# Kernel optimization log

Hardware: AMD Instinct MI355X
Metric: run time of the kernel (lower is better)

## Reference

```python
import jax, jax.numpy as jnp
import numpy as np

K = 16                 # nn_k neighbors (self excluded)
FILTER_SCALE = 2.0
SHARPNESS_SIGMA = 0.75
EPS = 1e-17


def _eps_denom(x):
    return jnp.where(x < EPS, EPS, x)


def _normalize(x):
    # F.normalize(dim=-1) semantics
    return x / jnp.maximum(jnp.linalg.norm(x, axis=-1, keepdims=True), 1e-12)


def _gather(feat, idx):
    # feat: (B,P,D), idx: (B,P,K) -> (B,P,K,D)   (== pytorch3d knn_gather)
    return jnp.take_along_axis(feat[:, None, :, :], idx[:, :, :, None], axis=2)


def _knn(points, k):
    # points: (B,P,3) -> squared dists (B,P,k), idxs (B,P,k); self excluded
    d2 = jnp.sum(points * points, axis=-1)
    dists = d2[:, :, None] + d2[:, None, :] - 2.0 * jnp.einsum('bpd,bqd->bpq', points, points)
    P = points.shape[1]
    r = jnp.arange(P)
    dists = dists.at[:, r, r].set(-jnp.inf)  # force self to be rank-0 of top_k
    neg, idx = jax.lax.top_k(-dists, k + 1)
    return jnp.maximum(-neg[:, :, 1:], 0.0), idx[:, :, 1:]


def _denoise(normals, idx, w):
    # weighted neighbor average of normals, per _denoise_normals
    nn_n = _gather(normals, idx)                       # (B,P,K,3)
    return jnp.sum(nn_n * w[..., None], axis=-2) / _eps_denom(
        jnp.sum(w, axis=-1, keepdims=True))


def setup_inputs() -> dict:
    key = jax.random.key(0)
    kp, kn = jax.random.split(key)
    B, P = 2, 8192
    points = jax.random.normal(kp, (B, P, 3), dtype=jnp.float32)
    normals = jax.random.normal(kn, (B, P, 3), dtype=jnp.float32)
    return {"points": points, "normals": normals}


def reference(points, normals):
    # --- torch.no_grad block: knn build + all weights + normal denoising ---
    pts_ng = jax.lax.stop_gradient(points)
    dists, idx = _knn(pts_ng, K)                       # (B,P,K)
    nn = _gather(pts_ng, idx)                          # (B,P,K,3), detached

    # phi = (1 - d/(2*d1*fs^2))^4, clamped at 0 (get_phi)
    s = dists[:, :, :1] * 2.0 * FILTER_SCALE * FILTER_SCALE
    w = jnp.maximum(1.0 - dists / _eps_denom(s), 0.0)
    phi = (w * w) * (w * w)

    n_ng = jax.lax.stop_gradient(normals)
    n1 = _denoise(n_ng, idx, phi)                      # first denoise with phi

    # normal_w = exp(-||n - ni||^2 / sigma^2) on normalized once-denoised normals
    nn_n = _gather(n1, idx)
    diff = _normalize(nn_n) - _normalize(n1)[:, :, None, :]
    inv_sigma = 1.0 / (SHARPNESS_SIGMA * SHARPNESS_SIGMA)
    normal_w = jnp.exp(-jnp.sum(diff * diff, axis=-1) * inv_sigma)

    # second denoise with phi * normal_w
    n2 = _denoise(n1, idx, phi * normal_w)

    # weights_proj = phi * spatial_w_proj(==1) * normal_w, ball-query masked
    weights_proj = phi * normal_w
    ball_mask = dists > FILTER_SCALE * dists[:, :, :1] * 2.0
    weights_proj = jnp.where(ball_mask, 0.0, weights_proj)
    weights_proj = jax.lax.stop_gradient(weights_proj)

    # --- outside no_grad: gather denoised normals, signed point-to-plane ---
    nn_normals = _gather(n2, idx)                      # (B,P,K,3) (no grad path)
    dist_to_surface = jnp.sum((nn - points[:, :, None, :]) * nn_normals, axis=-1)

    # projection loss: weighted mean of squared point-to-plane distance
    loss = jnp.sum(dist_to_surface * dist_to_surface * weights_proj, axis=-1) / \
        _eps_denom(jnp.sum(weights_proj, axis=-1))     # (B,P)
    return jnp.mean(loss)                              # BaseLoss reduction='mean'
```

## Files before the change

kernel.cpp:

```cpp
#include <hip/hip_runtime.h>
#include <math.h>

#define PP    8192
#define NB    2
#define NPTS  16384
#define KNN   16
#define EPSV  1e-17f
#define CH    128
#define NSUP  16
#define NCELL 4096

#define KEY_BIG 3.0e38f


__device__ __forceinline__ int spread3(int v) {
    return (v & 1) | ((v & 2) << 2) | ((v & 4) << 4) | ((v & 8) << 6);
}

__global__ __launch_bounds__(1024) void sort_kernel(
        const float* __restrict__ pts,
        float4* __restrict__ sorted4,
        int*    __restrict__ perm) {
    __shared__ int lh[NCELL];
    __shared__ int wtot[16];
    const int b = blockIdx.x;
    const int t = threadIdx.x;
    const int lane = t & 63, wid = t >> 6;
    const float* bp = pts + (size_t)b * PP * 3;

    for (int k = t; k < NCELL; k += 1024) lh[k] = 0;
    __syncthreads();

    float px[8], py[8], pz[8];
    int cell[8];
#pragma unroll
    for (int k = 0; k < 8; ++k) {
        const int p = t + k * 1024;
        const float x = bp[p * 3 + 0];
        const float y = bp[p * 3 + 1];
        const float z = bp[p * 3 + 2];
        px[k] = x; py[k] = y; pz[k] = z;
        const int ix = (int)fminf(fmaxf((x + 5.0f) * 1.6f, 0.0f), 15.0f);
        const int iy = (int)fminf(fmaxf((y + 5.0f) * 1.6f, 0.0f), 15.0f);
        const int iz = (int)fminf(fmaxf((z + 5.0f) * 1.6f, 0.0f), 15.0f);
        cell[k] = spread3(ix) | (spread3(iy) << 1) | (spread3(iz) << 2);
        atomicAdd(&lh[cell[k]], 1);
    }
    __syncthreads();

    const int v0 = lh[t * 4 + 0];
    const int v1 = lh[t * 4 + 1];
    const int v2 = lh[t * 4 + 2];
    const int v3 = lh[t * 4 + 3];
    const int s4 = v0 + v1 + v2 + v3;
    int v = s4;
#pragma unroll
    for (int off = 1; off < 64; off <<= 1) {
        int uu = __shfl_up(v, off, 64);
        if (lane >= off) v += uu;
    }
    if (lane == 63) wtot[wid] = v;
    __syncthreads();
    if (wid == 0) {
        int w = (lane < 16) ? wtot[lane] : 0;
#pragma unroll
        for (int off = 1; off < 16; off <<= 1) {
            int uu = __shfl_up(w, off, 64);
            if (lane >= off) w += uu;
        }
        if (lane < 16) wtot[lane] = w;
    }
    __syncthreads();
    const int wbase = (wid > 0) ? wtot[wid - 1] : 0;
    const int excl = wbase + v - s4;
    lh[t * 4 + 0] = excl;
    lh[t * 4 + 1] = excl + v0;
    lh[t * 4 + 2] = excl + v0 + v1;
    lh[t * 4 + 3] = excl + v0 + v1 + v2;
    __syncthreads();

#pragma unroll
    for (int k = 0; k < 8; ++k) {
        const int pos = atomicAdd(&lh[cell[k]], 1);
        sorted4[(size_t)b * PP + pos] =
            make_float4(px[k], py[k], pz[k],
                        px[k] * px[k] + py[k] * py[k] + pz[k] * pz[k]);
        perm[b * PP + pos] = t + k * 1024;
    }
}

__global__ void bbox_kernel(const float4* __restrict__ sorted4,
                            float4* __restrict__ bbmin,
                            float4* __restrict__ bbmax,
                            float4* __restrict__ sbmin,
                            float4* __restrict__ sbmax) {
    __shared__ float4 smn[8], smx[8];
    const int lane = threadIdx.x & 63;
    const int wave = threadIdx.x >> 6;
    const int cw = blockIdx.x * 8 + wave;
    const float4 v = sorted4[cw * 64 + lane];
    float mnx = v.x, mny = v.y, mnz = v.z;
    float mxx = v.x, mxy = v.y, mxz = v.z;
#pragma unroll
    for (int off = 32; off >= 1; off >>= 1) {
        mnx = fminf(mnx, __shfl_xor(mnx, off, 64));
        mny = fminf(mny, __shfl_xor(mny, off, 64));
        mnz = fminf(mnz, __shfl_xor(mnz, off, 64));
        mxx = fmaxf(mxx, __shfl_xor(mxx, off, 64));
        mxy = fmaxf(mxy, __shfl_xor(mxy, off, 64));
        mxz = fmaxf(mxz, __shfl_xor(mxz, off, 64));
    }
    if (lane == 0) {
        bbmin[cw] = make_float4(mnx, mny, mnz, 0.f);
        bbmax[cw] = make_float4(mxx, mxy, mxz, 0.f);
        smn[wave] = make_float4(mnx, mny, mnz, 0.f);
        smx[wave] = make_float4(mxx, mxy, mxz, 0.f);
    }
    __syncthreads();
    if (threadIdx.x == 0) {
        float4 a = smn[0], bmx = smx[0];
#pragma unroll
        for (int k = 1; k < 8; ++k) {
            a.x = fminf(a.x, smn[k].x); a.y = fminf(a.y, smn[k].y);
            a.z = fminf(a.z, smn[k].z);
            bmx.x = fmaxf(bmx.x, smx[k].x); bmx.y = fmaxf(bmx.y, smx[k].y);
            bmx.z = fmaxf(bmx.z, smx[k].z);
        }
        sbmin[blockIdx.x] = a;
        sbmax[blockIdx.x] = bmx;
    }
}

__device__ __forceinline__ void insert16(float (&keys)[KNN], float kk) {
#pragma unroll
    for (int s = KNN - 1; s >= 1; --s)
        keys[s] = __builtin_amdgcn_fmed3f(keys[s - 1], kk, keys[s]);
    keys[0] = fminf(keys[0], kk);
}

__device__ __forceinline__ void merge16(float (&a)[KNN], const float (&o)[KNN]) {
    float c[KNN];
#pragma unroll
    for (int s = 0; s < KNN; ++s) c[s] = fminf(a[s], o[KNN - 1 - s]);
#pragma unroll
    for (int st = KNN / 2; st >= 1; st >>= 1) {
#pragma unroll
        for (int base = 0; base < KNN; base += 2 * st) {
#pragma unroll
            for (int k = 0; k < st; ++k) {
                const float x = c[base + k], y = c[base + k + st];
                c[base + k]      = fminf(x, y);
                c[base + k + st] = fmaxf(x, y);
            }
        }
    }
#pragma unroll
    for (int s = 0; s < KNN; ++s) a[s] = c[s];
}

__global__ __launch_bounds__(256) void knn2_kernel(
        const float4* __restrict__ sorted4,
        const int*    __restrict__ perm,
        const float*  __restrict__ normals,
        const float4* __restrict__ bbmin,
        const float4* __restrict__ bbmax,
        const float4* __restrict__ sbmin,
        const float4* __restrict__ sbmax,
        int*   __restrict__ out_idx,
        float* __restrict__ out_phi,
        float* __restrict__ out_n1) {
    const int lane = threadIdx.x & 63;
    const int wv   = threadIdx.x >> 6;
    const int W    = blockIdx.x * 4 + wv;
    const int b    = W >> 12;
    const int qg   = W & 4095;
    const int qbase = qg * 2;
    const int i    = lane & 1;
    const int u    = lane >> 1;
    const int qloc = qbase + i;
    const int s0   = qbase >> 9;
    const float4* sb = sorted4 + (size_t)b * PP;
    const int bCH = b * CH;

    const float4 q4 = sb[qloc];
    const float qx = q4.x, qy = q4.y, qz = q4.z;
    const float d2q = qx * qx + qy * qy + qz * qz;

    float keys[KNN];
#pragma unroll
    for (int s = 0; s < KNN; ++s) keys[s] = KEY_BIG;

    auto proc = [&](int c) {
#pragma unroll
        for (int t = 0; t < 2; ++t) {
            const int j = c * 64 + u + 32 * t;
            const float4 c4 = sb[j];
            const float dot = fmaf(qz, c4.z, fmaf(qy, c4.y, qx * c4.x));
            const float d  = fmaf(-2.0f, dot, d2q + c4.w);
            const float dc = fmaxf(d, 0.0f);
            float kv = __uint_as_float(
                (__float_as_uint(dc) & 0xFFFFE000u) | (unsigned)j);
            if (j == qloc) kv = KEY_BIG;
            if (kv < keys[KNN - 1]) insert16(keys, kv);
        }
    };

    const int cb0 = s0 * 8;
    for (int k = 0; k < 8; ++k) proc(cb0 + k);

    unsigned Bq;
    {
        float tk[KNN];
#pragma unroll
        for (int s = 0; s < KNN; ++s) tk[s] = keys[s];
#pragma unroll
        for (int st = 0; st < 4; ++st) {
            const int S = 2 << st;
            float o[KNN];
#pragma unroll
            for (int s = 0; s < KNN; ++s) o[s] = __shfl_xor(tk[s], S, 64);
            merge16(tk, o);
        }
        float o15[KNN];
#pragma unroll
        for (int s = 0; s < KNN; ++s) o15[s] = __shfl_xor(tk[s], 32, 64);
        float B = fminf(tk[0], o15[KNN - 1]);
#pragma unroll
        for (int s = 1; s < KNN; ++s)
            B = fmaxf(B, fminf(tk[s], o15[KNN - 1 - s]));
        Bq = __float_as_uint(B);
    }

    {
        const int sup = (lane >> 2) & 15;
        const float4 smn = sbmin[b * NSUP + sup];
        const float4 smx = sbmax[b * NSUP + sup];
        const float ax = fmaxf(fmaxf(smn.x - qx, qx - smx.x), 0.0f);
        const float ay = fmaxf(fmaxf(smn.y - qy, qy - smx.y), 0.0f);
        const float az = fmaxf(fmaxf(smn.z - qz, qz - smx.z), 0.0f);
        const float dmS = (ax * ax + ay * ay + az * az) * 0.999999f;
        const unsigned flS = __float_as_uint(dmS) & 0xFFFFE000u;
        const unsigned long long M =
            __ballot((sup != s0) && (flS < Bq));

        for (int s = 0; s < NSUP; ++s) {
            if (!(M & (0xFULL << (s * 4)))) continue;
            const int cc = s * 8 + (u & 7);
            const float4 cmn = bbmin[bCH + cc];
            const float4 cmx = bbmax[bCH + cc];
            const float bx = fmaxf(fmaxf(cmn.x - qx, qx - cmx.x), 0.0f);
            const float by = fmaxf(fmaxf(cmn.y - qy, qy - cmx.y), 0.0f);
            const float bz = fmaxf(fmaxf(cmn.z - qz, qz - cmx.z), 0.0f);
            const float dmC = (bx * bx + by * by + bz * bz) * 0.999999f;
            const unsigned flC = __float_as_uint(dmC) & 0xFFFFE000u;
            const unsigned long long M2 = __ballot(flC < Bq);
#pragma unroll
            for (int k = 0; k < 8; ++k)
                if (M2 & (0x0003000300030003ULL << (2 * k))) proc(s * 8 + k);
        }
    }

#pragma unroll
    for (int st = 0; st < 5; ++st) {
        const int S = 2 << st;
        float o[KNN];
#pragma unroll
        for (int s = 0; s < KNN; ++s) o[s] = __shfl_xor(keys[s], S, 64);
        merge16(keys, o);
    }

    const int su = u & 15;
    float myk = keys[0];
#pragma unroll
    for (int s = 1; s < KNN; ++s) myk = (su == s) ? keys[s] : myk;
    const int j = (int)(__float_as_uint(myk) & 0x1FFFu);

    const float4 nb4 = sb[j];
    const float dot = fmaf(qz, nb4.z, fmaf(qy, nb4.y, qx * nb4.x));
    float dd = fmaf(-2.0f, dot, d2q + nb4.w);
    dd = fmaxf(dd, 0.0f);

    float d1 = dd;
#pragma unroll
    for (int st = 0; st < 4; ++st) d1 = fminf(d1, __shfl_xor(d1, 2 << st, 64));

    const float s0v  = d1 * 8.0f;
    const float sden = (s0v < EPSV) ? EPSV : s0v;
    const float w  = fmaxf(1.0f - dd / sden, 0.0f);
    const float ph = (w * w) * (w * w);

    const int qrow = (b << 13) + qloc;
    if (u < 16) {
        out_idx[qrow * KNN + u] = j;
        out_phi[qrow * KNN + u] = ph;
    }

    const float* bn = normals + (size_t)b * PP * 3;
    const int jo = perm[(b << 13) + j];
    const float nx = bn[jo * 3 + 0];
    const float ny = bn[jo * 3 + 1];
    const float nz = bn[jo * 3 + 2];
    float sx = ph * nx, sy = ph * ny, sz = ph * nz, ss = ph;
#pragma unroll
    for (int st = 0; st < 4; ++st) {
        const int S = 2 << st;
        sx += __shfl_xor(sx, S, 64);
        sy += __shfl_xor(sy, S, 64);
        sz += __shfl_xor(sz, S, 64);
        ss += __shfl_xor(ss, S, 64);
    }
    if (u == 0) {
        const float den = (ss < EPSV) ? EPSV : ss;
        out_n1[qrow * 3 + 0] = sx / den;
        out_n1[qrow * 3 + 1] = sy / den;
        out_n1[qrow * 3 + 2] = sz / den;
    }
}

__global__ __launch_bounds__(256) void denoise2_kernel(
        const int* __restrict__ idx,
        const float* __restrict__ phi,
        const float* __restrict__ n1,
        float* __restrict__ nw_out,
        float* __restrict__ n2_out) {
    const int gid = blockIdx.x * 256 + threadIdx.x;
    const int q = gid >> 4;
    const int s = gid & 15;
    const int b = q >> 13;
    const int gbase = b * PP;
    const float INV_SIG = 1.0f / (0.75f * 0.75f);

    const float ax = n1[q * 3 + 0];
    const float ay = n1[q * 3 + 1];
    const float az = n1[q * 3 + 2];
    const float an = fmaxf(sqrtf(ax * ax + ay * ay + az * az), 1e-12f);
    const float rx = ax / an, ry = ay / an, rz = az / an;

    const int j = idx[q * KNN + s];
    const float bx = n1[(gbase + j) * 3 + 0];
    const float by = n1[(gbase + j) * 3 + 1];
    const float bz = n1[(gbase + j) * 3 + 2];
    const float bnn = fmaxf(sqrtf(bx * bx + by * by + bz * bz), 1e-12f);
    const float ux = bx / bnn - rx;
    const float uy = by / bnn - ry;
    const float uz = bz / bnn - rz;
    const float dq = ux * ux + uy * uy + uz * uz;
    const float nw = expf(-dq * INV_SIG);
    nw_out[q * KNN + s] = nw;

    const float wk = phi[q * KNN + s] * nw;
    float ox = wk * bx, oy = wk * by, oz = wk * bz, swn = wk;
#pragma unroll
    for (int off = 1; off < 16; off <<= 1) {
        ox  += __shfl_xor(ox,  off, 64);
        oy  += __shfl_xor(oy,  off, 64);
        oz  += __shfl_xor(oz,  off, 64);
        swn += __shfl_xor(swn, off, 64);
    }
    if (s == 0) {
        const float den = (swn < EPSV) ? EPSV : swn;
        n2_out[q * 3 + 0] = ox / den;
        n2_out[q * 3 + 1] = oy / den;
        n2_out[q * 3 + 2] = oz / den;
    }
}

__global__ __launch_bounds__(256) void loss_kernel(
        const float4* __restrict__ sorted4,
        const int* __restrict__ idx,
        const float* __restrict__ phi,
        const float* __restrict__ nw,
        const float* __restrict__ n2,
        float* __restrict__ partial) {
    const int gid = blockIdx.x * 256 + threadIdx.x;
    const int q = gid >> 4;
    const int s = gid & 15;
    const int b = q >> 13;
    const int il = q & (PP - 1);
    const float4* sbp = sorted4 + (size_t)b * PP;
    const int gbase = b * PP;

    const float4 p4 = sbp[il];
    const float px = p4.x, py = p4.y, pz = p4.z;
    const float d2q = px * px + py * py + pz * pz;

    const int j = idx[q * KNN + s];
    const float4 nb4 = sbp[j];
    const float dot = fmaf(pz, nb4.z, fmaf(py, nb4.y, px * nb4.x));
    const float dv  = fmaf(-2.0f, dot, d2q + nb4.w);
    const float d   = fmaxf(dv, 0.0f);

    float d1 = d;
#pragma unroll
    for (int off = 1; off < 16; off <<= 1) d1 = fminf(d1, __shfl_xor(d1, off, 64));

    float w = phi[q * KNN + s] * nw[q * KNN + s];
    if (d > 4.0f * d1) w = 0.f;

    const float nx = n2[(gbase + j) * 3 + 0];
    const float ny = n2[(gbase + j) * 3 + 1];
    const float nz = n2[(gbase + j) * 3 + 2];
    const float dts = (nb4.x - px) * nx +
                      (nb4.y - py) * ny +
                      (nb4.z - pz) * nz;
    float num = dts * dts * w, den = w;
#pragma unroll
    for (int off = 1; off < 16; off <<= 1) {
        num += __shfl_xor(num, off, 64);
        den += __shfl_xor(den, off, 64);
    }

    __shared__ float ls[16];
    if (s == 0) {
        const float dd = (den < EPSV) ? EPSV : den;
        ls[threadIdx.x >> 4] = num / dd;
    }
    __syncthreads();
    if (threadIdx.x == 0) {
        float v = 0.f;
#pragma unroll
        for (int k = 0; k < 16; ++k) v += ls[k];
        partial[blockIdx.x] = v;
    }
}

__global__ void finalize_kernel(const float* __restrict__ partial,
                                float* __restrict__ out) {
    float v = 0.f;
#pragma unroll
    for (int k = 0; k < 16; ++k) v += partial[threadIdx.x + 64 * k];
#pragma unroll
    for (int off = 32; off >= 1; off >>= 1) v += __shfl_down(v, off, 64);
    if (threadIdx.x == 0) out[0] = v / (float)NPTS;
}

extern "C" void kernel_launch(void* const* d_in, const int* in_sizes, int n_in,
                              void* d_out, int out_size, void* d_ws, size_t ws_size,
                              hipStream_t stream) {
    const float* points  = (const float*)d_in[0];
    const float* normals = (const float*)d_in[1];
    float* out = (float*)d_out;

    float* wsf    = (float*)d_ws;
    int*   w_idx  = (int*)wsf;
    float* w_phi  = wsf + 262144;
    float* w_nw   = wsf + 524288;
    float* w_n1   = wsf + 786432;
    float* w_n2   = wsf + 835584;
    float4* w_sorted4 = (float4*)(wsf + 884736);
    float* w_part = wsf + 950272;
    int*    w_perm   = (int*)(wsf + 524288);
    float4* w_bbmin  = (float4*)(wsf + 557056);
    float4* w_bbmax  = (float4*)(wsf + 558080);
    float4* w_sbmin  = (float4*)(wsf + 559104);
    float4* w_sbmax  = (float4*)(wsf + 559232);

    sort_kernel   <<<NB, 1024, 0, stream>>>(points, w_sorted4, w_perm);
    bbox_kernel   <<<32, 512, 0, stream>>>(w_sorted4, w_bbmin, w_bbmax,
                                           w_sbmin, w_sbmax);
    knn2_kernel   <<<2048, 256, 0, stream>>>(w_sorted4, w_perm, normals,
                                             w_bbmin, w_bbmax, w_sbmin, w_sbmax,
                                             w_idx, w_phi, w_n1);
    denoise2_kernel<<<1024, 256, 0, stream>>>(w_idx, w_phi, w_n1, w_nw, w_n2);
    loss_kernel   <<<1024, 256, 0, stream>>>(w_sorted4, w_idx, w_phi, w_nw, w_n2, w_part);
    finalize_kernel<<<1, 64, 0, stream>>>(w_part, out);
}
```

Before: 133.6 us.

## Merge seed top-k early and share ring candidates via ballot; fuse final reduction with atomics

The KNN kernel now fully merges the per-lane top-16 lists right after the seed cells, so every lane holds the exact current 16th-nearest bound. Ring cells then use a wave ballot and shuffle to broadcast each qualifying candidate into the shared sorted list. This tightens pruning and drops the separate final merge, at the cost of a serialized per-candidate insertion loop. Separately, the finalize kernel is removed and the loss kernel accumulates into the output with atomicAdd after a memset, which makes the float summation order nondeterministic.

```diff
diff --git a/kernel.cpp b/kernel.cpp
--- a/kernel.cpp
+++ b/kernel.cpp
@@ -190,7 +190,7 @@
 #pragma unroll
     for (int s = 0; s < KNN; ++s) keys[s] = KEY_BIG;
 
-    auto proc = [&](int c) {
+    auto proc_seed = [&](int c) {
 #pragma unroll
         for (int t = 0; t < 2; ++t) {
             const int j = c * 64 + u + 32 * t;
@@ -205,30 +205,38 @@
         }
     };
 
+    auto proc_ring = [&](int c) {
+#pragma unroll
+        for (int t = 0; t < 2; ++t) {
+            const int j = c * 64 + u + 32 * t;
+            const float4 c4 = sb[j];
+            const float dot = fmaf(qz, c4.z, fmaf(qy, c4.y, qx * c4.x));
+            const float d  = fmaf(-2.0f, dot, d2q + c4.w);
+            const float dc = fmaxf(d, 0.0f);
+            float kv = __uint_as_float(
+                (__float_as_uint(dc) & 0xFFFFE000u) | (unsigned)j);
+            if (j == qloc) kv = KEY_BIG;
+            unsigned long long am = __ballot(kv < keys[KNN - 1]);
+            while (am) {
+                const int src = __ffsll(am) - 1;
+                am &= am - 1;
+                const float kb = __shfl(kv, src, 64);
+                if ((lane & 1) == (src & 1))
+                    insert16(keys, kb);
+            }
+        }
+    };
+
     const int cb0 = s0 * 8;
-    for (int k = 0; k < 8; ++k) proc(cb0 + k);
-
-    unsigned Bq;
-    {
-        float tk[KNN];
-#pragma unroll
-        for (int s = 0; s < KNN; ++s) tk[s] = keys[s];
-#pragma unroll
-        for (int st = 0; st < 4; ++st) {
-            const int S = 2 << st;
-            float o[KNN];
-#pragma unroll
-            for (int s = 0; s < KNN; ++s) o[s] = __shfl_xor(tk[s], S, 64);
-            merge16(tk, o);
-        }
-        float o15[KNN];
-#pragma unroll
-        for (int s = 0; s < KNN; ++s) o15[s] = __shfl_xor(tk[s], 32, 64);
-        float B = fminf(tk[0], o15[KNN - 1]);
-#pragma unroll
-        for (int s = 1; s < KNN; ++s)
-            B = fmaxf(B, fminf(tk[s], o15[KNN - 1 - s]));
-        Bq = __float_as_uint(B);
+    for (int k = 0; k < 8; ++k) proc_seed(cb0 + k);
+
+#pragma unroll
+    for (int st = 0; st < 5; ++st) {
+        const int S = 2 << st;
+        float o[KNN];
+#pragma unroll
+        for (int s = 0; s < KNN; ++s) o[s] = __shfl_xor(keys[s], S, 64);
+        merge16(keys, o);
     }
 
     {
@@ -241,7 +249,7 @@
         const float dmS = (ax * ax + ay * ay + az * az) * 0.999999f;
         const unsigned flS = __float_as_uint(dmS) & 0xFFFFE000u;
         const unsigned long long M =
-            __ballot((sup != s0) && (flS < Bq));
+            __ballot((sup != s0) && (flS < __float_as_uint(keys[KNN - 1])));
 
         for (int s = 0; s < NSUP; ++s) {
             if (!(M & (0xFULL << (s * 4)))) continue;
@@ -253,20 +261,12 @@
             const float bz = fmaxf(fmaxf(cmn.z - qz, qz - cmx.z), 0.0f);
             const float dmC = (bx * bx + by * by + bz * bz) * 0.999999f;
             const unsigned flC = __float_as_uint(dmC) & 0xFFFFE000u;
-            const unsigned long long M2 = __ballot(flC < Bq);
+            const unsigned long long M2 =
+                __ballot(flC < __float_as_uint(keys[KNN - 1]));
 #pragma unroll
             for (int k = 0; k < 8; ++k)
-                if (M2 & (0x0003000300030003ULL << (2 * k))) proc(s * 8 + k);
-        }
-    }
-
-#pragma unroll
-    for (int st = 0; st < 5; ++st) {
-        const int S = 2 << st;
-        float o[KNN];
-#pragma unroll
-        for (int s = 0; s < KNN; ++s) o[s] = __shfl_xor(keys[s], S, 64);
-        merge16(keys, o);
+                if (M2 & (0x0003000300030003ULL << (2 * k))) proc_ring(s * 8 + k);
+        }
     }
 
     const int su = u & 15;
@@ -371,7 +371,7 @@
         const float* __restrict__ phi,
         const float* __restrict__ nw,
         const float* __restrict__ n2,
-        float* __restrict__ partial) {
+        float* __restrict__ out) {
     const int gid = blockIdx.x * 256 + threadIdx.x;
     const int q = gid >> 4;
     const int s = gid & 15;
@@ -420,18 +420,8 @@
         float v = 0.f;
 #pragma unroll
         for (int k = 0; k < 16; ++k) v += ls[k];
-        partial[blockIdx.x] = v;
-    }
-}
-
-__global__ void finalize_kernel(const float* __restrict__ partial,
-                                float* __restrict__ out) {
-    float v = 0.f;
-#pragma unroll
-    for (int k = 0; k < 16; ++k) v += partial[threadIdx.x + 64 * k];
-#pragma unroll
-    for (int off = 32; off >= 1; off >>= 1) v += __shfl_down(v, off, 64);
-    if (threadIdx.x == 0) out[0] = v / (float)NPTS;
+        atomicAdd(out, v * (1.0f / (float)NPTS));
+    }
 }
 
 extern "C" void kernel_launch(void* const* d_in, const int* in_sizes, int n_in,
@@ -448,13 +438,13 @@
     float* w_n1   = wsf + 786432;
     float* w_n2   = wsf + 835584;
     float4* w_sorted4 = (float4*)(wsf + 884736);
-    float* w_part = wsf + 950272;
     int*    w_perm   = (int*)(wsf + 524288);
     float4* w_bbmin  = (float4*)(wsf + 557056);
     float4* w_bbmax  = (float4*)(wsf + 558080);
     float4* w_sbmin  = (float4*)(wsf + 559104);
     float4* w_sbmax  = (float4*)(wsf + 559232);
 
+    hipMemsetAsync(out, 0, sizeof(float), stream);
     sort_kernel   <<<NB, 1024, 0, stream>>>(points, w_sorted4, w_perm);
     bbox_kernel   <<<32, 512, 0, stream>>>(w_sorted4, w_bbmin, w_bbmax,
                                            w_sbmin, w_sbmax);
@@ -462,6 +452,5 @@
                                              w_bbmin, w_bbmax, w_sbmin, w_sbmax,
                                              w_idx, w_phi, w_n1);
     denoise2_kernel<<<1024, 256, 0, stream>>>(w_idx, w_phi, w_n1, w_nw, w_n2);
-    loss_kernel   <<<1024, 256, 0, stream>>>(w_sorted4, w_idx, w_phi, w_nw, w_n2, w_part);
-    finalize_kernel<<<1, 64, 0, stream>>>(w_part, out);
-}
+    loss_kernel   <<<1024, 256, 0, stream>>>(w_sorted4, w_idx, w_phi, w_nw, w_n2, out);
+}
```

After: 159.7 us. +19.6%, slower.

## Assign one query per wavefront in KNN kernel instead of two

Applied to the files above, without the earlier changes.

The KNN kernel now maps each 64-lane wavefront to a single query rather than two interleaved queries. Each lane handles one candidate per cell chunk, and the merge trees, ballot masks and reductions are rewritten for one query per wave. This doubles the wavefront count and halves the sequential candidate work per lane, giving more parallelism and per-query culling. In exchange there is an extra shuffle-merge stage and twice as many box tests and merges in total.

```diff
diff --git a/kernel.cpp b/kernel.cpp
--- a/kernel.cpp
+++ b/kernel.cpp
@@ -158,7 +158,7 @@
     for (int s = 0; s < KNN; ++s) a[s] = c[s];
 }
 
-__global__ __launch_bounds__(256) void knn2_kernel(
+__global__ __launch_bounds__(256) void knn1_kernel(
         const float4* __restrict__ sorted4,
         const int*    __restrict__ perm,
         const float*  __restrict__ normals,
@@ -172,13 +172,9 @@
     const int lane = threadIdx.x & 63;
     const int wv   = threadIdx.x >> 6;
     const int W    = blockIdx.x * 4 + wv;
-    const int b    = W >> 12;
-    const int qg   = W & 4095;
-    const int qbase = qg * 2;
-    const int i    = lane & 1;
-    const int u    = lane >> 1;
-    const int qloc = qbase + i;
-    const int s0   = qbase >> 9;
+    const int b    = W >> 13;
+    const int qloc = W & (PP - 1);
+    const int s0   = qloc >> 9;
     const float4* sb = sorted4 + (size_t)b * PP;
     const int bCH = b * CH;
 
@@ -191,18 +187,15 @@
     for (int s = 0; s < KNN; ++s) keys[s] = KEY_BIG;
 
     auto proc = [&](int c) {
-#pragma unroll
-        for (int t = 0; t < 2; ++t) {
-            const int j = c * 64 + u + 32 * t;
-            const float4 c4 = sb[j];
-            const float dot = fmaf(qz, c4.z, fmaf(qy, c4.y, qx * c4.x));
-            const float d  = fmaf(-2.0f, dot, d2q + c4.w);
-            const float dc = fmaxf(d, 0.0f);
-            float kv = __uint_as_float(
-                (__float_as_uint(dc) & 0xFFFFE000u) | (unsigned)j);
-            if (j == qloc) kv = KEY_BIG;
-            if (kv < keys[KNN - 1]) insert16(keys, kv);
-        }
+        const int j = c * 64 + lane;
+        const float4 c4 = sb[j];
+        const float dot = fmaf(qz, c4.z, fmaf(qy, c4.y, qx * c4.x));
+        const float d  = fmaf(-2.0f, dot, d2q + c4.w);
+        const float dc = fmaxf(d, 0.0f);
+        float kv = __uint_as_float(
+            (__float_as_uint(dc) & 0xFFFFE000u) | (unsigned)j);
+        if (j == qloc) kv = KEY_BIG;
+        if (kv < keys[KNN - 1]) insert16(keys, kv);
     };
 
     const int cb0 = s0 * 8;
@@ -214,8 +207,8 @@
 #pragma unroll
         for (int s = 0; s < KNN; ++s) tk[s] = keys[s];
 #pragma unroll
-        for (int st = 0; st < 4; ++st) {
-            const int S = 2 << st;
+        for (int st = 0; st < 5; ++st) {
+            const int S = 1 << st;
             float o[KNN];
 #pragma unroll
             for (int s = 0; s < KNN; ++s) o[s] = __shfl_xor(tk[s], S, 64);
@@ -232,20 +225,19 @@
     }
 
     {
-        const int sup = (lane >> 2) & 15;
-        const float4 smn = sbmin[b * NSUP + sup];
-        const float4 smx = sbmax[b * NSUP + sup];
+        const float4 smn = sbmin[b * NSUP + (lane & 15)];
+        const float4 smx = sbmax[b * NSUP + (lane & 15)];
         const float ax = fmaxf(fmaxf(smn.x - qx, qx - smx.x), 0.0f);
         const float ay = fmaxf(fmaxf(smn.y - qy, qy - smx.y), 0.0f);
         const float az = fmaxf(fmaxf(smn.z - qz, qz - smx.z), 0.0f);
         const float dmS = (ax * ax + ay * ay + az * az) * 0.999999f;
         const unsigned flS = __float_as_uint(dmS) & 0xFFFFE000u;
         const unsigned long long M =
-            __ballot((sup != s0) && (flS < Bq));
+            __ballot((lane < 16) && ((lane & 15) != s0) && (flS < Bq));
 
         for (int s = 0; s < NSUP; ++s) {
-            if (!(M & (0xFULL << (s * 4)))) continue;
-            const int cc = s * 8 + (u & 7);
+            if (!(M & (1ULL << s))) continue;
+            const int cc = s * 8 + (lane & 7);
             const float4 cmn = bbmin[bCH + cc];
             const float4 cmx = bbmax[bCH + cc];
             const float bx = fmaxf(fmaxf(cmn.x - qx, qx - cmx.x), 0.0f);
@@ -253,23 +245,23 @@
             const float bz = fmaxf(fmaxf(cmn.z - qz, qz - cmx.z), 0.0f);
             const float dmC = (bx * bx + by * by + bz * bz) * 0.999999f;
             const unsigned flC = __float_as_uint(dmC) & 0xFFFFE000u;
-            const unsigned long long M2 = __ballot(flC < Bq);
+            const unsigned long long M2 = __ballot((lane < 8) && (flC < Bq));
 #pragma unroll
             for (int k = 0; k < 8; ++k)
-                if (M2 & (0x0003000300030003ULL << (2 * k))) proc(s * 8 + k);
+                if (M2 & (1ULL << k)) proc(s * 8 + k);
         }
     }
 
 #pragma unroll
-    for (int st = 0; st < 5; ++st) {
-        const int S = 2 << st;
+    for (int st = 0; st < 6; ++st) {
+        const int S = 1 << st;
         float o[KNN];
 #pragma unroll
         for (int s = 0; s < KNN; ++s) o[s] = __shfl_xor(keys[s], S, 64);
         merge16(keys, o);
     }
 
-    const int su = u & 15;
+    const int su = lane & 15;
     float myk = keys[0];
 #pragma unroll
     for (int s = 1; s < KNN; ++s) myk = (su == s) ? keys[s] : myk;
@@ -282,7 +274,7 @@
 
     float d1 = dd;
 #pragma unroll
-    for (int st = 0; st < 4; ++st) d1 = fminf(d1, __shfl_xor(d1, 2 << st, 64));
+    for (int st = 0; st < 4; ++st) d1 = fminf(d1, __shfl_xor(d1, 1 << st, 64));
 
     const float s0v  = d1 * 8.0f;
     const float sden = (s0v < EPSV) ? EPSV : s0v;
@@ -290,9 +282,9 @@
     const float ph = (w * w) * (w * w);
 
     const int qrow = (b << 13) + qloc;
-    if (u < 16) {
-        out_idx[qrow * KNN + u] = j;
-        out_phi[qrow * KNN + u] = ph;
+    if (lane < 16) {
+        out_idx[qrow * KNN + lane] = j;
+        out_phi[qrow * KNN + lane] = ph;
     }
 
     const float* bn = normals + (size_t)b * PP * 3;
@@ -303,13 +295,13 @@
     float sx = ph * nx, sy = ph * ny, sz = ph * nz, ss = ph;
 #pragma unroll
     for (int st = 0; st < 4; ++st) {
-        const int S = 2 << st;
+        const int S = 1 << st;
         sx += __shfl_xor(sx, S, 64);
         sy += __shfl_xor(sy, S, 64);
         sz += __shfl_xor(sz, S, 64);
         ss += __shfl_xor(ss, S, 64);
     }
-    if (u == 0) {
+    if (lane == 0) {
         const float den = (ss < EPSV) ? EPSV : ss;
         out_n1[qrow * 3 + 0] = sx / den;
         out_n1[qrow * 3 + 1] = sy / den;
@@ -458,7 +450,7 @@
     sort_kernel   <<<NB, 1024, 0, stream>>>(points, w_sorted4, w_perm);
     bbox_kernel   <<<32, 512, 0, stream>>>(w_sorted4, w_bbmin, w_bbmax,
                                            w_sbmin, w_sbmax);
-    knn2_kernel   <<<2048, 256, 0, stream>>>(w_sorted4, w_perm, normals,
+    knn1_kernel   <<<4096, 256, 0, stream>>>(w_sorted4, w_perm, normals,
                                              w_bbmin, w_bbmax, w_sbmin, w_sbmax,
                                              w_idx, w_phi, w_n1);
     denoise2_kernel<<<1024, 256, 0, stream>>>(w_idx, w_phi, w_n1, w_nw, w_n2);
```

New measurement: 139.3 us. 4.3% more time.
